# Performance work log

Measured on AMD Instinct MI355X. Metric: run time of the kernel, lower is better.

## Reference

```python
import jax, jax.numpy as jnp
import numpy as np

A_BITS = 16
W_BITS = 8
KH = KW = 3
STRIDE = 1
PADDING = 1


def fake_quant(x, bits, axes=None):
    """Asymmetric min/max fake quantization with straight-through estimator."""
    if axes is None:
        mn = x.min()
        mx = x.max()
    else:
        mn = x.min(axis=axes, keepdims=True)
        mx = x.max(axis=axes, keepdims=True)
    qmax = float(2 ** bits - 1)
    scale = jnp.maximum((mx - mn) / qmax, 1e-12)
    zp = jnp.round(-mn / scale)
    q = jnp.clip(jnp.round(x / scale) + zp, 0.0, qmax)
    deq = (q - zp) * scale
    # STE: identity gradient through the quantizer
    return x + jax.lax.stop_gradient(deq - x)


def unfold(x, kh, kw, stride, padding):
    """torch.nn.functional.unfold equivalent -> (N, C*kh*kw, Hout*Wout)."""
    N, C, H, W = x.shape
    xp = jnp.pad(x, ((0, 0), (0, 0), (padding, padding), (padding, padding)))
    Ho = (H - kh + 2 * padding) // stride + 1
    Wo = (W - kw + 2 * padding) // stride + 1
    cols = []
    for i in range(kh):          # small fixed 3x3 loop
        for j in range(kw):
            cols.append(xp[:, :, i:i + Ho * stride:stride, j:j + Wo * stride:stride])
    xcol = jnp.stack(cols, axis=2)              # (N, C, kh*kw, Ho, Wo)
    return xcol.reshape(N, C * kh * kw, Ho * Wo), Ho, Wo


def adder_op(W_col, X_col):
    # W_col: (F, K), X_col: (K, L) -> out: (F, L); L1-distance "conv"
    return -jnp.abs(W_col[:, :, None] - X_col[None, :, :]).sum(axis=1)


def setup_inputs() -> dict:
    key = jax.random.key(0)
    kx, kw = jax.random.split(key)
    x = jax.random.normal(kx, (4, 64, 28, 28), dtype=jnp.float32)
    W = jax.random.normal(kw, (64, 64, 3, 3), dtype=jnp.float32)
    return {"x": x, "W": W}


def reference(x, W):
    # first_layer == 0 -> activation fake-quant; per-channel weight fake-quant
    qx = fake_quant(x, A_BITS)
    qw = fake_quant(W, W_BITS, axes=(1, 2, 3))
    N = x.shape[0]
    F = W.shape[0]
    xcol, Ho, Wo = unfold(qx, KH, KW, STRIDE, PADDING)   # (N, K, L0)
    K = xcol.shape[1]
    # torch: permute(1,2,0).view(K, L0*N) -> batch fastest within a row
    X_col = jnp.transpose(xcol, (1, 2, 0)).reshape(K, -1)  # (K, L0*N)
    W_col = qw.reshape(F, K)
    out = adder_op(W_col, X_col)                            # (F, L0*N)
    out = out.reshape(F, Ho, Wo, N).transpose(3, 0, 1, 2)   # (N, F, Ho, Wo)
    return out
```

## Files before the change

### kernel.cpp

```cpp
#include <hip/hip_runtime.h>
#include <math.h>

#define N_  4
#define C_  64
#define H_  28
#define W_  28
#define F_  64
#define KK  576
#define NX  (N_*C_*H_*W_)
#define NX4 (NX/4)

#define XCH 52


__global__ __launch_bounds__(256) void k_prep(const float* __restrict__ x,
                                              const float* __restrict__ Wg,
                                              float* __restrict__ ws) {
  __shared__ float sm[4], sM[4];
  int tid = threadIdx.x, lane = tid & 63, wv = tid >> 6;

  const float4* x4 = (const float4*)x;
  int gid = blockIdx.x * 256 + tid;
  float m = 3.4e38f, M = -3.4e38f;
  if (gid < NX4) {
    float4 v = x4[gid];
    m = fminf(fminf(v.x, v.y), fminf(v.z, v.w));
    M = fmaxf(fmaxf(v.x, v.y), fmaxf(v.z, v.w));
  }
  #pragma unroll
  for (int o = 32; o; o >>= 1) {
    m = fminf(m, __shfl_xor(m, o));
    M = fmaxf(M, __shfl_xor(M, o));
  }
  if (lane == 0) { sm[wv] = m; sM[wv] = M; }
  __syncthreads();
  if (tid == 0) {
    m = fminf(fminf(sm[0], sm[1]), fminf(sm[2], sm[3]));
    M = fmaxf(fmaxf(sM[0], sM[1]), fmaxf(sM[2], sM[3]));
    ws[blockIdx.x] = m;
    ws[256 + blockIdx.x] = M;
  }

  if (blockIdx.x < 16) {
    int f = blockIdx.x * 4 + wv;
    const float* wp = Wg + f * KK;
    float v[9];
    float wm = 3.4e38f, wM = -3.4e38f;
    #pragma unroll
    for (int u = 0; u < 9; ++u) {
      v[u] = wp[lane + 64 * u];
      wm = fminf(wm, v[u]);
      wM = fmaxf(wM, v[u]);
    }
    #pragma unroll
    for (int o = 32; o; o >>= 1) {
      wm = fminf(wm, __shfl_xor(wm, o));
      wM = fmaxf(wM, __shfl_xor(wM, o));
    }
    float s = fmaxf((wM - wm) / 255.0f, 1e-12f);
    float z = rintf(-wm / s);
    float rs = 1.0f / s;
    float* Wt = ws + 512;
    #pragma unroll
    for (int u = 0; u < 9; ++u) {
      float q = fminf(fmaxf(rintf(v[u] * rs) + z, 0.0f), 255.0f);
      Wt[(lane + 64 * u) * 64 + f] = (q - z) * s;
    }
  }
}

__global__ __launch_bounds__(256, 2) void k_main(const float* __restrict__ x,
                                                 const float* __restrict__ ws,
                                                 float* __restrict__ out) {
  __shared__ __align__(16) float Xs[64 * XCH];
  __shared__ float Rbuf[16 * 32 * 15];
  int tid = threadIdx.x;
  int lane = tid & 63;
  int fl = tid & 15, cq = tid >> 4;
  int y = blockIdx.x, n = blockIdx.y;
  int fh = blockIdx.z >> 1, colh = blockIdx.z & 1;
  int bc = colh * 14;

  const float4* mp = (const float4*)ws;
  float4 mv = mp[lane], Mv = mp[64 + lane];
  float m = fminf(fminf(mv.x, mv.y), fminf(mv.z, mv.w));
  float M = fmaxf(fmaxf(Mv.x, Mv.y), fmaxf(Mv.z, Mv.w));
  #pragma unroll
  for (int o = 32; o; o >>= 1) {
    m = fminf(m, __shfl_xor(m, o));
    M = fmaxf(M, __shfl_xor(M, o));
  }
  float sx = fmaxf((M - m) / 65535.0f, 1e-12f);
  float zx = rintf(-m / sx);
  float rx = 1.0f / sx;

  {
    int j = tid & 15, sub = tid >> 4;
    #pragma unroll
    for (int it = 0; it < 12; ++it) {
      int cr = sub + 16 * it;
      int c = cr / 3, r = cr - c * 3;
      int row = y + r - 1, col = bc - 1 + j;
      float v = 0.0f;
      if ((unsigned)row < 28u && (unsigned)col < 28u) {
        float raw = x[((n * 64 + c) * 28 + row) * 28 + col];
        float q = fminf(fmaxf(rintf(raw * rx) + zx, 0.0f), 65535.0f);
        v = (q - zx) * sx;
      }
      Xs[c * XCH + r * 16 + j] = v;
    }
  }
  __syncthreads();

  const float* Wt = ws + 512;
  int f0 = fh * 32 + fl;
  float acc0[14], acc1[14];
  #pragma unroll
  for (int i = 0; i < 14; ++i) { acc0[i] = 0.0f; acc1[i] = 0.0f; }

  float wc[18], wn[18];
  {
    const float* wp = Wt + (cq * 9) * 64 + f0;
    #pragma unroll
    for (int k = 0; k < 9; ++k) { wn[k] = wp[k * 64]; wn[9 + k] = wp[k * 64 + 16]; }
  }

  for (int ci = 0; ci < 4; ++ci) {
    #pragma unroll
    for (int k = 0; k < 18; ++k) wc[k] = wn[k];
    if (ci < 3) {
      const float* wp = Wt + ((cq + 16 * (ci + 1)) * 9) * 64 + f0;
      #pragma unroll
      for (int k = 0; k < 9; ++k) { wn[k] = wp[k * 64]; wn[9 + k] = wp[k * 64 + 16]; }
    }
    int c = cq + 16 * ci;
    #pragma unroll
    for (int r = 0; r < 3; ++r) {
      const float4* xr4 = (const float4*)&Xs[c * XCH + r * 16];
      float xv[16];
      #pragma unroll
      for (int i = 0; i < 4; ++i) ((float4*)xv)[i] = xr4[i];
      float wa0 = wc[3 * r], wa1 = wc[3 * r + 1], wa2 = wc[3 * r + 2];
      float wb0 = wc[9 + 3 * r], wb1 = wc[9 + 3 * r + 1], wb2 = wc[9 + 3 * r + 2];
      #pragma unroll
      for (int p = 0; p < 14; ++p) {
        acc0[p] += fabsf(wa0 - xv[p]) + fabsf(wa1 - xv[p + 1]) + fabsf(wa2 - xv[p + 2]);
        acc1[p] += fabsf(wb0 - xv[p]) + fabsf(wb1 - xv[p + 1]) + fabsf(wb2 - xv[p + 2]);
      }
    }
  }

  #pragma unroll
  for (int p = 0; p < 14; ++p) {
    Rbuf[(cq * 32 + fl) * 15 + p]      = acc0[p];
    Rbuf[(cq * 32 + 16 + fl) * 15 + p] = acc1[p];
  }
  __syncthreads();

  #pragma unroll
  for (int i = 0; i < 2; ++i) {
    int idx = tid + 256 * i;
    if (idx < 448) {
      int ff = idx / 14, col = idx - ff * 14;
      float s = 0.0f;
      #pragma unroll
      for (int q = 0; q < 16; ++q) s += Rbuf[(q * 32 + ff) * 15 + col];
      out[((n * 64 + fh * 32 + ff) * 28 + y) * 28 + bc + col] = -s;
    }
  }
}

extern "C" void kernel_launch(void* const* d_in, const int* in_sizes, int n_in,
                              void* d_out, int out_size, void* d_ws, size_t ws_size,
                              hipStream_t stream) {
  const float* x  = (const float*)d_in[0];
  const float* Wg = (const float*)d_in[1];
  float* out = (float*)d_out;
  float* ws  = (float*)d_ws;

  hipLaunchKernelGGL(k_prep, dim3(256), dim3(256), 0, stream, x, Wg, ws);
  hipLaunchKernelGGL(k_main, dim3(28, 4, 4), dim3(256), 0, stream, x, ws, out);
}
```

Baseline: 73.10 us.

## Fuse prep and main kernels into one cooperative launch with grid sync

Replaces the two-kernel sequence with a single cooperative kernel of 448 blocks. Each block computes a partial activation min/max (and the first 16 blocks quantize the weights), then prefetches its raw input tile into registers before a grid-wide sync. After the sync the tile is quantized from those registers. This removes one kernel launch and overlaps the input load with the reduction, at the cost of a grid barrier and a cooperative-launch requirement; if the cooperative launch fails, the code falls back to the original two kernels.

```diff
diff --git a/kernel.cpp b/kernel.cpp
--- a/kernel.cpp
+++ b/kernel.cpp
@@ -1,5 +1,8 @@
 #include <hip/hip_runtime.h>
+#include <hip/hip_cooperative_groups.h>
 #include <math.h>
+
+namespace cg = cooperative_groups;
 
 #define N_  4
 #define C_  64
@@ -9,9 +12,10 @@
 #define KK  576
 #define NX  (N_*C_*H_*W_)
 #define NX4 (NX/4)
+#define NBLK 448
+#define PER_BLK (NX4/NBLK)
 
 #define XCH 52
-
 
 __global__ __launch_bounds__(256) void k_prep(const float* __restrict__ x,
                                               const float* __restrict__ Wg,
@@ -170,6 +174,178 @@
   }
 }
 
+__global__ __launch_bounds__(256, 2) void k_fused(const float* __restrict__ x,
+                                                  const float* __restrict__ Wg,
+                                                  float* __restrict__ ws,
+                                                  float* __restrict__ out) {
+  __shared__ __align__(16) float Xs[64 * XCH];
+  __shared__ float Rbuf[16 * 32 * 15];
+  __shared__ float sm[4], sM[4];
+
+  int tid = threadIdx.x;
+  int lane = tid & 63, wv = tid >> 6;
+  int fl = tid & 15, cq = tid >> 4;
+
+  int b = blockIdx.x;
+  int y = b % 28;
+  int rest = b / 28;
+  int n = rest & 3;
+  int z = rest >> 2;
+  int fh = z >> 1, colh = z & 1;
+  int bc = colh * 14;
+
+  const float4* x4 = (const float4*)x;
+  float m = 3.4e38f, M = -3.4e38f;
+  if (tid < PER_BLK) {
+    float4 v = x4[b * PER_BLK + tid];
+    m = fminf(fminf(v.x, v.y), fminf(v.z, v.w));
+    M = fmaxf(fmaxf(v.x, v.y), fmaxf(v.z, v.w));
+  }
+  #pragma unroll
+  for (int o = 32; o; o >>= 1) {
+    m = fminf(m, __shfl_xor(m, o));
+    M = fmaxf(M, __shfl_xor(M, o));
+  }
+  if (lane == 0) { sm[wv] = m; sM[wv] = M; }
+  __syncthreads();
+  if (tid == 0) {
+    ws[b]       = fminf(fminf(sm[0], sm[1]), fminf(sm[2], sm[3]));
+    ws[512 + b] = fmaxf(fmaxf(sM[0], sM[1]), fmaxf(sM[2], sM[3]));
+  }
+
+  if (b < 16) {
+    int f = b * 4 + wv;
+    const float* wp = Wg + f * KK;
+    float v[9];
+    float wm = 3.4e38f, wM = -3.4e38f;
+    #pragma unroll
+    for (int u = 0; u < 9; ++u) {
+      v[u] = wp[lane + 64 * u];
+      wm = fminf(wm, v[u]);
+      wM = fmaxf(wM, v[u]);
+    }
+    #pragma unroll
+    for (int o = 32; o; o >>= 1) {
+      wm = fminf(wm, __shfl_xor(wm, o));
+      wM = fmaxf(wM, __shfl_xor(wM, o));
+    }
+    float s = fmaxf((wM - wm) / 255.0f, 1e-12f);
+    float z2 = rintf(-wm / s);
+    float rs = 1.0f / s;
+    float* Wt = ws + 1024;
+    #pragma unroll
+    for (int u = 0; u < 9; ++u) {
+      float q = fminf(fmaxf(rintf(v[u] * rs) + z2, 0.0f), 255.0f);
+      Wt[(lane + 64 * u) * 64 + f] = (q - z2) * s;
+    }
+  }
+
+  float xr[12];
+  {
+    int j = tid & 15, sub = tid >> 4;
+    #pragma unroll
+    for (int it = 0; it < 12; ++it) {
+      int cr = sub + 16 * it;
+      int c = cr / 3, r = cr - c * 3;
+      int row = y + r - 1, col = bc - 1 + j;
+      xr[it] = ((unsigned)row < 28u && (unsigned)col < 28u)
+                 ? x[((n * 64 + c) * 28 + row) * 28 + col] : 0.0f;
+    }
+  }
+
+  __threadfence();
+  cg::this_grid().sync();
+
+  float pm = 3.4e38f, pM = -3.4e38f;
+  #pragma unroll
+  for (int i = 0; i < 7; ++i) {
+    pm = fminf(pm, ws[lane + 64 * i]);
+    pM = fmaxf(pM, ws[512 + lane + 64 * i]);
+  }
+  #pragma unroll
+  for (int o = 32; o; o >>= 1) {
+    pm = fminf(pm, __shfl_xor(pm, o));
+    pM = fmaxf(pM, __shfl_xor(pM, o));
+  }
+  float sx = fmaxf((pM - pm) / 65535.0f, 1e-12f);
+  float zx = rintf(-pm / sx);
+  float rx = 1.0f / sx;
+
+  {
+    int j = tid & 15, sub = tid >> 4;
+    #pragma unroll
+    for (int it = 0; it < 12; ++it) {
+      int cr = sub + 16 * it;
+      int c = cr / 3, r = cr - c * 3;
+      int row = y + r - 1, col = bc - 1 + j;
+      float v = 0.0f;
+      if ((unsigned)row < 28u && (unsigned)col < 28u) {
+        float q = fminf(fmaxf(rintf(xr[it] * rx) + zx, 0.0f), 65535.0f);
+        v = (q - zx) * sx;
+      }
+      Xs[c * XCH + r * 16 + j] = v;
+    }
+  }
+  __syncthreads();
+
+  const float* Wt = ws + 1024;
+  int f0 = fh * 32 + fl;
+  float acc0[14], acc1[14];
+  #pragma unroll
+  for (int i = 0; i < 14; ++i) { acc0[i] = 0.0f; acc1[i] = 0.0f; }
+
+  float wc[18], wn[18];
+  {
+    const float* wp = Wt + (cq * 9) * 64 + f0;
+    #pragma unroll
+    for (int k = 0; k < 9; ++k) { wn[k] = wp[k * 64]; wn[9 + k] = wp[k * 64 + 16]; }
+  }
+
+  for (int ci = 0; ci < 4; ++ci) {
+    #pragma unroll
+    for (int k = 0; k < 18; ++k) wc[k] = wn[k];
+    if (ci < 3) {
+      const float* wp = Wt + ((cq + 16 * (ci + 1)) * 9) * 64 + f0;
+      #pragma unroll
+      for (int k = 0; k < 9; ++k) { wn[k] = wp[k * 64]; wn[9 + k] = wp[k * 64 + 16]; }
+    }
+    int c = cq + 16 * ci;
+    #pragma unroll
+    for (int r = 0; r < 3; ++r) {
+      const float4* xr4 = (const float4*)&Xs[c * XCH + r * 16];
+      float xv[16];
+      #pragma unroll
+      for (int i = 0; i < 4; ++i) ((float4*)xv)[i] = xr4[i];
+      float wa0 = wc[3 * r], wa1 = wc[3 * r + 1], wa2 = wc[3 * r + 2];
+      float wb0 = wc[9 + 3 * r], wb1 = wc[9 + 3 * r + 1], wb2 = wc[9 + 3 * r + 2];
+      #pragma unroll
+      for (int p = 0; p < 14; ++p) {
+        acc0[p] += fabsf(wa0 - xv[p]) + fabsf(wa1 - xv[p + 1]) + fabsf(wa2 - xv[p + 2]);
+        acc1[p] += fabsf(wb0 - xv[p]) + fabsf(wb1 - xv[p + 1]) + fabsf(wb2 - xv[p + 2]);
+      }
+    }
+  }
+
+  #pragma unroll
+  for (int p = 0; p < 14; ++p) {
+    Rbuf[(cq * 32 + fl) * 15 + p]      = acc0[p];
+    Rbuf[(cq * 32 + 16 + fl) * 15 + p] = acc1[p];
+  }
+  __syncthreads();
+
+  #pragma unroll
+  for (int i = 0; i < 2; ++i) {
+    int idx = tid + 256 * i;
+    if (idx < 448) {
+      int ff = idx / 14, col = idx - ff * 14;
+      float s = 0.0f;
+      #pragma unroll
+      for (int q = 0; q < 16; ++q) s += Rbuf[(q * 32 + ff) * 15 + col];
+      out[((n * 64 + fh * 32 + ff) * 28 + y) * 28 + bc + col] = -s;
+    }
+  }
+}
+
 extern "C" void kernel_launch(void* const* d_in, const int* in_sizes, int n_in,
                               void* d_out, int out_size, void* d_ws, size_t ws_size,
                               hipStream_t stream) {
@@ -178,6 +354,12 @@
   float* out = (float*)d_out;
   float* ws  = (float*)d_ws;
 
-  hipLaunchKernelGGL(k_prep, dim3(256), dim3(256), 0, stream, x, Wg, ws);
-  hipLaunchKernelGGL(k_main, dim3(28, 4, 4), dim3(256), 0, stream, x, ws, out);
+  void* args[] = {(void*)&x, (void*)&Wg, (void*)&ws, (void*)&out};
+  hipError_t e = hipLaunchCooperativeKernel((const void*)k_fused, dim3(NBLK),
+                                            dim3(256), args, 0, stream);
+  if (e != hipSuccess) {
+    (void)hipGetLastError();
+    hipLaunchKernelGGL(k_prep, dim3(256), dim3(256), 0, stream, x, Wg, ws);
+    hipLaunchKernelGGL(k_main, dim3(28, 4, 4), dim3(256), 0, stream, x, ws, out);
+  }
 }
```

After: 183.1 us. 2.51x slower.

## Split output columns into quarters and prefetch input before min/max reduction

Applied to the files above, without the earlier changes.

Each block of the main kernel now covers 7 output columns instead of 14, which doubles the grid to 896 blocks and halves the per-thread accumulators and the shared-memory footprint. The raw input halo tile is loaded into registers before the activation min/max reduction is read, so global load latency can overlap that reduction. Quantized values are written to shared memory afterwards. The cost is more halo overlap (9 input columns loaded per 7 outputs) and fewer outputs per weight load, so weight reuse from the workspace drops.

```diff
diff --git a/kernel.cpp b/kernel.cpp
--- a/kernel.cpp
+++ b/kernel.cpp
@@ -10,7 +10,7 @@
 #define NX  (N_*C_*H_*W_)
 #define NX4 (NX/4)
 
-#define XCH 52
+#define XCH 40
 
 
 __global__ __launch_bounds__(256) void k_prep(const float* __restrict__ x,
@@ -73,13 +73,28 @@
                                                  const float* __restrict__ ws,
                                                  float* __restrict__ out) {
   __shared__ __align__(16) float Xs[64 * XCH];
-  __shared__ float Rbuf[16 * 32 * 15];
+  __shared__ float Rbuf[16 * 32 * 9];
   int tid = threadIdx.x;
   int lane = tid & 63;
   int fl = tid & 15, cq = tid >> 4;
   int y = blockIdx.x, n = blockIdx.y;
-  int fh = blockIdx.z >> 1, colh = blockIdx.z & 1;
-  int bc = colh * 14;
+  int fh = blockIdx.z >> 2, colq = blockIdx.z & 3;
+  int bc = colq * 7;
+
+  float xr[7];
+  #pragma unroll
+  for (int it = 0; it < 7; ++it) {
+    int e = tid + 256 * it;
+    float v = 0.0f;
+    if (e < 1728) {
+      int c = e / 27, rem = e - c * 27;
+      int r = rem / 9, j = rem - r * 9;
+      int row = y + r - 1, col = bc - 1 + j;
+      if ((unsigned)row < 28u && (unsigned)col < 28u)
+        v = x[((n * 64 + c) * 28 + row) * 28 + col];
+    }
+    xr[it] = v;
+  }
 
   const float4* mp = (const float4*)ws;
   float4 mv = mp[lane], Mv = mp[64 + lane];
@@ -94,29 +109,23 @@
   float zx = rintf(-m / sx);
   float rx = 1.0f / sx;
 
-  {
-    int j = tid & 15, sub = tid >> 4;
-    #pragma unroll
-    for (int it = 0; it < 12; ++it) {
-      int cr = sub + 16 * it;
-      int c = cr / 3, r = cr - c * 3;
-      int row = y + r - 1, col = bc - 1 + j;
-      float v = 0.0f;
-      if ((unsigned)row < 28u && (unsigned)col < 28u) {
-        float raw = x[((n * 64 + c) * 28 + row) * 28 + col];
-        float q = fminf(fmaxf(rintf(raw * rx) + zx, 0.0f), 65535.0f);
-        v = (q - zx) * sx;
-      }
-      Xs[c * XCH + r * 16 + j] = v;
+  #pragma unroll
+  for (int it = 0; it < 7; ++it) {
+    int e = tid + 256 * it;
+    if (e < 1728) {
+      int c = e / 27, rem = e - c * 27;
+      int r = rem / 9, j = rem - r * 9;
+      float q = fminf(fmaxf(rintf(xr[it] * rx) + zx, 0.0f), 65535.0f);
+      Xs[c * XCH + r * 12 + j] = (q - zx) * sx;
     }
   }
   __syncthreads();
 
   const float* Wt = ws + 512;
   int f0 = fh * 32 + fl;
-  float acc0[14], acc1[14];
+  float acc0[7], acc1[7];
   #pragma unroll
-  for (int i = 0; i < 14; ++i) { acc0[i] = 0.0f; acc1[i] = 0.0f; }
+  for (int i = 0; i < 7; ++i) { acc0[i] = 0.0f; acc1[i] = 0.0f; }
 
   float wc[18], wn[18];
   {
@@ -136,14 +145,14 @@
     int c = cq + 16 * ci;
     #pragma unroll
     for (int r = 0; r < 3; ++r) {
-      const float4* xr4 = (const float4*)&Xs[c * XCH + r * 16];
-      float xv[16];
+      const float4* xp = (const float4*)&Xs[c * XCH + r * 12];
+      float xv[12];
       #pragma unroll
-      for (int i = 0; i < 4; ++i) ((float4*)xv)[i] = xr4[i];
+      for (int i = 0; i < 3; ++i) ((float4*)xv)[i] = xp[i];
       float wa0 = wc[3 * r], wa1 = wc[3 * r + 1], wa2 = wc[3 * r + 2];
       float wb0 = wc[9 + 3 * r], wb1 = wc[9 + 3 * r + 1], wb2 = wc[9 + 3 * r + 2];
       #pragma unroll
-      for (int p = 0; p < 14; ++p) {
+      for (int p = 0; p < 7; ++p) {
         acc0[p] += fabsf(wa0 - xv[p]) + fabsf(wa1 - xv[p + 1]) + fabsf(wa2 - xv[p + 2]);
         acc1[p] += fabsf(wb0 - xv[p]) + fabsf(wb1 - xv[p + 1]) + fabsf(wb2 - xv[p + 2]);
       }
@@ -151,22 +160,18 @@
   }
 
   #pragma unroll
-  for (int p = 0; p < 14; ++p) {
-    Rbuf[(cq * 32 + fl) * 15 + p]      = acc0[p];
-    Rbuf[(cq * 32 + 16 + fl) * 15 + p] = acc1[p];
+  for (int p = 0; p < 7; ++p) {
+    Rbuf[(cq * 32 + fl) * 9 + p]      = acc0[p];
+    Rbuf[(cq * 32 + 16 + fl) * 9 + p] = acc1[p];
   }
   __syncthreads();
 
-  #pragma unroll
-  for (int i = 0; i < 2; ++i) {
-    int idx = tid + 256 * i;
-    if (idx < 448) {
-      int ff = idx / 14, col = idx - ff * 14;
-      float s = 0.0f;
-      #pragma unroll
-      for (int q = 0; q < 16; ++q) s += Rbuf[(q * 32 + ff) * 15 + col];
-      out[((n * 64 + fh * 32 + ff) * 28 + y) * 28 + bc + col] = -s;
-    }
+  if (tid < 224) {
+    int ff = tid / 7, col = tid - ff * 7;
+    float s = 0.0f;
+    #pragma unroll
+    for (int q = 0; q < 16; ++q) s += Rbuf[(q * 32 + ff) * 9 + col];
+    out[((n * 64 + fh * 32 + ff) * 28 + y) * 28 + bc + col] = -s;
   }
 }
 
@@ -179,5 +184,5 @@
   float* ws  = (float*)d_ws;
 
   hipLaunchKernelGGL(k_prep, dim3(256), dim3(256), 0, stream, x, Wg, ws);
-  hipLaunchKernelGGL(k_main, dim3(28, 4, 4), dim3(256), 0, stream, x, ws, out);
+  hipLaunchKernelGGL(k_main, dim3(28, 4, 8), dim3(256), 0, stream, x, ws, out);
 }
```

Result: no change. 72.77 us (-0.5%).
